# Performance work log

Measured on AMD Instinct MI355X. Metric: run time of the kernel, lower is better.

The kernel has to match this reference:

```python
import jax, jax.numpy as jnp
import numpy as np
import math

B, S, HID, H = 2, 1024, 512, 8
D = HID // H  # 64
EPS = 1e-24


def setup_inputs() -> dict:
    key = jax.random.key(0)
    ks = jax.random.split(key, 12)
    s = 0.02
    return {
        "input_tensor": jax.random.normal(ks[0], (B, S, HID), dtype=jnp.float32),
        "attention_mask": jnp.zeros((B, 1, S, S), dtype=jnp.float32),
        # Linear weights stored as [in, out] (y = x @ W + b)
        "Wq": jax.random.normal(ks[1], (HID, HID), dtype=jnp.float32) * s,
        "bq": jnp.zeros((HID,), dtype=jnp.float32),
        "Wk": jax.random.normal(ks[2], (HID, HID), dtype=jnp.float32) * s,
        "bk": jnp.zeros((HID,), dtype=jnp.float32),
        "Wv": jax.random.normal(ks[3], (HID, HID), dtype=jnp.float32) * s,
        "bv": jnp.zeros((HID,), dtype=jnp.float32),
        # order_affine: Linear(2*D, 1)
        "order_w": jax.random.normal(ks[4], (2 * D,), dtype=jnp.float32) * s,
        "order_b": jnp.zeros((), dtype=jnp.float32),
        # distance_affine: Linear(2*D, 1)
        "dist_w": jax.random.normal(ks[5], (2 * D,), dtype=jnp.float32) * s,
        "dist_b": jnp.zeros((), dtype=jnp.float32),
        "scalar": jax.random.normal(ks[6], (1,), dtype=jnp.float32),
    }


def _heads(x):  # [B,S,HID] -> [B,H,S,D]
    return x.reshape(B, S, H, D).transpose(0, 2, 1, 3)


def reference(input_tensor, attention_mask, Wq, bq, Wk, bk, Wv, bv,
              order_w, order_b, dist_w, dist_b, scalar):
    scale = math.sqrt(D)

    mixed_q = input_tensor @ Wq + bq            # [B,S,HID]
    mixed_k = input_tensor @ Wk + bk
    mixed_v = input_tensor @ Wv + bv

    qh = _heads(mixed_q)                        # [B,H,S,D]
    kh = _heads(mixed_k)
    vh = _heads(mixed_v)

    scores = jnp.einsum('bhid,bhjd->bhij', qh, kh)   # [B,H,S,S]
    origin_scores = scores

    # --- order bias: sigmoid(affine(cat(q_i, k_j))) decomposed (same math,
    # avoids materializing the [B,H,S,S,2D] concat the torch code builds) ---
    q_ord = jnp.einsum('bhid,d->bhi', qh, order_w[:D])    # [B,H,S]
    k_ord = jnp.einsum('bhjd,d->bhj', kh, order_w[D:])
    pr_order = jax.nn.sigmoid(q_ord[..., :, None] + k_ord[..., None, :] + order_b)
    gd_order = jnp.triu(jnp.ones((S, S), dtype=scores.dtype), k=1)  # 1 where j>i
    error_order = (jnp.log(pr_order + EPS) * gd_order
                   + jnp.log(1.0 - pr_order + EPS) * (1.0 - gd_order))

    # --- distance bias ---
    idx = jnp.arange(S)
    gd_distance = jnp.log(jnp.abs(idx[None, :] - idx[:, None]).astype(scores.dtype) + 1.0)
    q_dst = jnp.einsum('bhid,d->bhi', qh, dist_w[:D])
    k_dst = jnp.einsum('bhjd,d->bhj', kh, dist_w[D:])
    pr_distance = q_dst[..., :, None] + k_dst[..., None, :] + dist_b   # [B,H,S,S]
    error_distance = -jnp.square(gd_distance - pr_distance) * jnp.square(scalar[0]) * 0.5

    adj_scores = scores + error_order + error_distance

    def _probs(sc):
        return jax.nn.softmax(sc / scale + attention_mask, axis=-1)

    attention_probs = _probs(adj_scores)
    origin_attention_probs = _probs(origin_scores)

    return (mixed_q, mixed_k, vh, attention_probs, origin_attention_probs)
```

## Files before the change

### kernel.cpp

```cpp
#include <hip/hip_runtime.h>
#include <math.h>

#define Sdim 1024
#define HIDdim 512
#define Hnum 8
#define Ddim 64

typedef __attribute__((ext_vector_type(4))) float f32x4;
typedef __attribute__((ext_vector_type(8))) short short8;
typedef __attribute__((ext_vector_type(4))) unsigned short ushort4v;

static __device__ __forceinline__ unsigned short f2bf(float x) {
    union { float f; unsigned u; } v; v.f = x;
    unsigned r = v.u + 0x7fffu + ((v.u >> 16) & 1u);
    return (unsigned short)(r >> 16);
}

__global__ __launch_bounds__(256) void qkv_gemm(
    const float* __restrict__ X,
    const float* __restrict__ Wq, const float* __restrict__ bq,
    const float* __restrict__ Wk, const float* __restrict__ bk,
    const float* __restrict__ Wv, const float* __restrict__ bv,
    float* __restrict__ outq, float* __restrict__ outk, float* __restrict__ outv)
{
    __shared__ unsigned short Ws[64][72];
    __shared__ unsigned short Xs[64][72];

    const int mb = blockIdx.x;
    const int nb = blockIdx.y;
    const int which = nb >> 3;
    const int n0 = (nb & 7) * 64;
    const float* __restrict__ W    = (which == 0) ? Wq : (which == 1) ? Wk : Wv;
    const float* __restrict__ bias = (which == 0) ? bq : (which == 1) ? bk : bv;

    const int t    = threadIdx.x;
    const int lane = t & 63;
    const int w    = t >> 6;
    const int g    = lane >> 4;
    const int c    = lane & 15;
    const int m0r  = mb * 64;

    f32x4 acc[4];
#pragma unroll
    for (int f = 0; f < 4; ++f) { f32x4 z = {0.f, 0.f, 0.f, 0.f}; acc[f] = z; }

    for (int kt = 0; kt < 512; kt += 64) {
        __syncthreads();
        {
            const int row = t >> 2, kb = (t & 3) * 16;
            const float* __restrict__ src = &X[(size_t)(m0r + row) * HIDdim + kt + kb];
#pragma unroll
            for (int i = 0; i < 4; ++i) {
                const f32x4 v = *(const f32x4*)&src[4 * i];
                ushort4v p;
                p.x = f2bf(v.x); p.y = f2bf(v.y); p.z = f2bf(v.z); p.w = f2bf(v.w);
                *(ushort4v*)&Xs[row][kb + 4 * i] = p;
            }
        }
#pragma unroll
        for (int p = 0; p < 4; ++p) {
            const int kr   = p * 16 + (t >> 4);
            const int nloc = (t & 15) * 4;
            const f32x4 v = *(const f32x4*)&W[(size_t)(kt + kr) * HIDdim + n0 + nloc];
            Ws[nloc + 0][kr] = f2bf(v.x);
            Ws[nloc + 1][kr] = f2bf(v.y);
            Ws[nloc + 2][kr] = f2bf(v.z);
            Ws[nloc + 3][kr] = f2bf(v.w);
        }
        __syncthreads();
        const short8 a0 = *(const short8*)&Ws[w * 16 + c][g * 8];
        const short8 a1 = *(const short8*)&Ws[w * 16 + c][32 + g * 8];
#pragma unroll
        for (int f = 0; f < 4; ++f) {
            const short8 b0 = *(const short8*)&Xs[f * 16 + c][g * 8];
            const short8 b1 = *(const short8*)&Xs[f * 16 + c][32 + g * 8];
            acc[f] = __builtin_amdgcn_mfma_f32_16x16x32_bf16(a0, b0, acc[f], 0, 0, 0);
            acc[f] = __builtin_amdgcn_mfma_f32_16x16x32_bf16(a1, b1, acc[f], 0, 0, 0);
        }
    }

    const int nql = w * 16 + g * 4;
    const f32x4 bb = *(const f32x4*)&bias[n0 + nql];
#pragma unroll
    for (int f = 0; f < 4; ++f) {
        const int m = m0r + f * 16 + c;
        f32x4 v = acc[f] + bb;
        if (which == 2) {
            const int b = m >> 10, s = m & 1023;
            const int h = nb & 7;
            *(f32x4*)&outv[((((size_t)b * Hnum + h) * Sdim) + s) * Ddim + nql] = v;
        } else {
            float* __restrict__ o = (which == 0) ? outq : outk;
            *(f32x4*)&o[(size_t)m * HIDdim + n0 + nql] = v;
        }
    }
}

__global__ __launch_bounds__(256) void prep_kernel(
    const float* __restrict__ mq, const float* __restrict__ mk,
    const float* __restrict__ order_w, const float* __restrict__ dist_w,
    unsigned short* __restrict__ qbf, unsigned short* __restrict__ kbf,
    float* __restrict__ qog, float* __restrict__ qdg,
    float* __restrict__ kog, float* __restrict__ kdg)
{
    const int tg  = blockIdx.x * 256 + threadIdx.x;
    const int row = tg >> 3;
    const int dc8 = (tg & 7) * 8;
    const int bh  = row >> 10, s = row & 1023;
    const int b   = bh >> 3,   h = bh & 7;
    const size_t src = ((size_t)b * Sdim + s) * HIDdim + h * Ddim + dc8;

    const f32x4 ow0 = *(const f32x4*)&order_w[dc8];
    const f32x4 ow1 = *(const f32x4*)&order_w[dc8 + 4];
    const f32x4 dw0 = *(const f32x4*)&dist_w[dc8];
    const f32x4 dw1 = *(const f32x4*)&dist_w[dc8 + 4];
    const f32x4 owk0 = *(const f32x4*)&order_w[Ddim + dc8];
    const f32x4 owk1 = *(const f32x4*)&order_w[Ddim + dc8 + 4];
    const f32x4 dwk0 = *(const f32x4*)&dist_w[Ddim + dc8];
    const f32x4 dwk1 = *(const f32x4*)&dist_w[Ddim + dc8 + 4];

    {
        const f32x4 v0 = *(const f32x4*)&mq[src];
        const f32x4 v1 = *(const f32x4*)&mq[src + 4];
        float po = v0.x * ow0.x + v0.y * ow0.y + v0.z * ow0.z + v0.w * ow0.w
                 + v1.x * ow1.x + v1.y * ow1.y + v1.z * ow1.z + v1.w * ow1.w;
        float pd = v0.x * dw0.x + v0.y * dw0.y + v0.z * dw0.z + v0.w * dw0.w
                 + v1.x * dw1.x + v1.y * dw1.y + v1.z * dw1.z + v1.w * dw1.w;
#pragma unroll
        for (int o = 1; o < 8; o <<= 1) { po += __shfl_xor(po, o); pd += __shfl_xor(pd, o); }
        if ((tg & 7) == 0) { qog[row] = po; qdg[row] = pd; }
        ushort4v p0, p1;
        p0.x = f2bf(v0.x); p0.y = f2bf(v0.y); p0.z = f2bf(v0.z); p0.w = f2bf(v0.w);
        p1.x = f2bf(v1.x); p1.y = f2bf(v1.y); p1.z = f2bf(v1.z); p1.w = f2bf(v1.w);
        *(ushort4v*)&qbf[(size_t)row * Ddim + dc8]     = p0;
        *(ushort4v*)&qbf[(size_t)row * Ddim + dc8 + 4] = p1;
    }
    {
        const f32x4 v0 = *(const f32x4*)&mk[src];
        const f32x4 v1 = *(const f32x4*)&mk[src + 4];
        float po = v0.x * owk0.x + v0.y * owk0.y + v0.z * owk0.z + v0.w * owk0.w
                 + v1.x * owk1.x + v1.y * owk1.y + v1.z * owk1.z + v1.w * owk1.w;
        float pd = v0.x * dwk0.x + v0.y * dwk0.y + v0.z * dwk0.z + v0.w * dwk0.w
                 + v1.x * dwk1.x + v1.y * dwk1.y + v1.z * dwk1.z + v1.w * dwk1.w;
#pragma unroll
        for (int o = 1; o < 8; o <<= 1) { po += __shfl_xor(po, o); pd += __shfl_xor(pd, o); }
        if ((tg & 7) == 0) { kog[row] = po; kdg[row] = pd; }
        ushort4v p0, p1;
        p0.x = f2bf(v0.x); p0.y = f2bf(v0.y); p0.z = f2bf(v0.z); p0.w = f2bf(v0.w);
        p1.x = f2bf(v1.x); p1.y = f2bf(v1.y); p1.z = f2bf(v1.z); p1.w = f2bf(v1.w);
        *(ushort4v*)&kbf[(size_t)row * Ddim + dc8]     = p0;
        *(ushort4v*)&kbf[(size_t)row * Ddim + dc8 + 4] = p1;
    }
}

__global__ __launch_bounds__(512, 6) void attn_kernel(
    const unsigned short* __restrict__ qbf, const unsigned short* __restrict__ kbf,
    const float* __restrict__ qog, const float* __restrict__ qdg,
    const float* __restrict__ kog, const float* __restrict__ kdg,
    const float* __restrict__ mask,
    const float* __restrict__ order_b_p, const float* __restrict__ dist_b_p,
    const float* __restrict__ scalar_p,
    float* __restrict__ out_adj, float* __restrict__ out_orig)
{
    __shared__ float ps[16][524];
    __shared__ float gdl[Sdim];
    __shared__ float red_s[16][8];

    const int t    = threadIdx.x;
    const int lane = t & 63;
    const int w    = t >> 6;
    const int g    = lane >> 4;
    const int c    = lane & 15;

    const int blk = blockIdx.x;
    const int ib  = blk & 63;
    const int bh  = blk >> 6;
    const int b   = bh >> 3;
    const int i0  = ib * 16;
    const int i   = i0 + c;

    const float order_b = order_b_p[0];
    const float dist_b  = dist_b_p[0];
    const float sc      = scalar_p[0];
    const float sc2h    = 0.5f * sc * sc;
    const float mscale  = 0.125f;

    {
        const int idx = t * 2;
        gdl[idx]     = __logf((float)idx + 1.0f);
        gdl[idx + 1] = __logf((float)idx + 2.0f);
    }
    __syncthreads();

    const size_t hbase = (size_t)bh * Sdim;
    const size_t qrow  = (hbase + i) * Ddim;
    const short8 qf0 = *(const short8*)&qbf[qrow + g * 8];
    const short8 qf1 = *(const short8*)&qbf[qrow + 32 + g * 8];

    f32x4 acc[8];
#pragma unroll
    for (int it = 0; it < 8; ++it) { f32x4 z = {0.f, 0.f, 0.f, 0.f}; acc[it] = z; }

#pragma unroll
    for (int it = 0; it < 8; ++it) {
        const size_t kr = (hbase + it * 128 + w * 16 + c) * Ddim;
        const short8 kf0 = *(const short8*)&kbf[kr + g * 8];
        const short8 kf1 = *(const short8*)&kbf[kr + 32 + g * 8];
        acc[it] = __builtin_amdgcn_mfma_f32_16x16x32_bf16(kf0, qf0, acc[it], 0, 0, 0);
        acc[it] = __builtin_amdgcn_mfma_f32_16x16x32_bf16(kf1, qf1, acc[it], 0, 0, 0);
    }

    const size_t obase = (size_t)bh * Sdim * Sdim;
    const float* __restrict__ mrow = &mask[((size_t)b * Sdim + i) * Sdim];

    float s0 = 0.0f;
#pragma unroll
    for (int it = 0; it < 8; ++it) {
        const int j0 = it * 128 + w * 16 + g * 4;
        const f32x4 mk4 = *(const f32x4*)&mrow[j0];
        f32x4 e;
#pragma unroll
        for (int r = 0; r < 4; ++r) e[r] = __expf(fmaf(acc[it][r], mscale, mk4[r]));
        acc[it] = e;
        s0 += e[0] + e[1] + e[2] + e[3];
    }
    s0 += __shfl_xor(s0, 16);
    s0 += __shfl_xor(s0, 32);
    if (lane < 16) red_s[lane][w] = s0;
    __syncthreads();
    f32x4 ra = *(const f32x4*)&red_s[c][0];
    f32x4 rb = *(const f32x4*)&red_s[c][4];
    const float inv0 = __builtin_amdgcn_rcpf(ra[0] + ra[1] + ra[2] + ra[3]
                                           + rb[0] + rb[1] + rb[2] + rb[3]);

#pragma unroll
    for (int hf = 0; hf < 2; ++hf) {
        __syncthreads();
#pragma unroll
        for (int it = 0; it < 4; ++it) {
            const int colw = it * 128 + w * 16 + g * 4;
            f32x4 p = acc[hf * 4 + it] * inv0;
            *(f32x4*)&ps[c][colw] = p;
        }
        __syncthreads();
        float* __restrict__ dst = out_orig + obase + (size_t)i0 * Sdim + hf * 512;
#pragma unroll
        for (int n = 0; n < 4; ++n) {
            const int row = 2 * w + (n >> 1);
            const int col = (n & 1) * 256 + lane * 4;
            const f32x4 v = *(const f32x4*)&ps[row][col];
            *(f32x4*)&dst[(size_t)row * Sdim + col] = v;
        }
    }

    const float qo = qog[hbase + i] + order_b;
    const float qd = qdg[hbase + i] + dist_b;
    float s1 = 0.0f;
#pragma unroll
    for (int it = 0; it < 8; ++it) {
        const int j0 = it * 128 + w * 16 + g * 4;
        const f32x4 ko4 = *(const f32x4*)&kog[hbase + j0];
        const f32x4 kd4 = *(const f32x4*)&kdg[hbase + j0];
        f32x4 p = acc[it];
#pragma unroll
        for (int r = 0; r < 4; ++r) {
            const int j = j0 + r;
            const float z    = qo + ko4[r];
            const float targ = (j > i) ? -z : z;
            const float u    = 1.0f + __expf(targ);
            const int   dl   = (i > j) ? (i - j) : (j - i);
            const float df   = gdl[dl] - (qd + kd4[r]);
            const float eD   = __expf(-0.125f * fmaf(sc2h * df, df, __logf(u)));
            p[r] *= eD;
            s1 += p[r];
        }
        acc[it] = p;
    }
    s1 += __shfl_xor(s1, 16);
    s1 += __shfl_xor(s1, 32);
    __syncthreads();
    if (lane < 16) red_s[lane][w] = s1;
    __syncthreads();
    ra = *(const f32x4*)&red_s[c][0];
    rb = *(const f32x4*)&red_s[c][4];
    const float inv1 = __builtin_amdgcn_rcpf(ra[0] + ra[1] + ra[2] + ra[3]
                                           + rb[0] + rb[1] + rb[2] + rb[3]);

#pragma unroll
    for (int hf = 0; hf < 2; ++hf) {
        __syncthreads();
#pragma unroll
        for (int it = 0; it < 4; ++it) {
            const int colw = it * 128 + w * 16 + g * 4;
            f32x4 p = acc[hf * 4 + it] * inv1;
            *(f32x4*)&ps[c][colw] = p;
        }
        __syncthreads();
        float* __restrict__ dst = out_adj + obase + (size_t)i0 * Sdim + hf * 512;
#pragma unroll
        for (int n = 0; n < 4; ++n) {
            const int row = 2 * w + (n >> 1);
            const int col = (n & 1) * 256 + lane * 4;
            const f32x4 v = *(const f32x4*)&ps[row][col];
            *(f32x4*)&dst[(size_t)row * Sdim + col] = v;
        }
    }
}

extern "C" void kernel_launch(void* const* d_in, const int* in_sizes, int n_in,
                              void* d_out, int out_size, void* d_ws, size_t ws_size,
                              hipStream_t stream) {
    const float* X    = (const float*)d_in[0];
    const float* mask = (const float*)d_in[1];
    const float* Wq   = (const float*)d_in[2];
    const float* bq   = (const float*)d_in[3];
    const float* Wk   = (const float*)d_in[4];
    const float* bk   = (const float*)d_in[5];
    const float* Wv   = (const float*)d_in[6];
    const float* bv   = (const float*)d_in[7];
    const float* ow   = (const float*)d_in[8];
    const float* ob   = (const float*)d_in[9];
    const float* dw   = (const float*)d_in[10];
    const float* db   = (const float*)d_in[11];
    const float* sc   = (const float*)d_in[12];

    float* out     = (float*)d_out;
    float* outq    = out;
    float* outk    = out + 1048576;
    float* outv    = out + 2097152;
    float* outadj  = out + 3145728;
    float* outorig = out + 19922944;

    unsigned short* qbf = (unsigned short*)d_ws;
    unsigned short* kbf = qbf + 16384 * 64;
    float* qog = (float*)(kbf + 16384 * 64);
    float* qdg = qog + 16384;
    float* kog = qdg + 16384;
    float* kdg = kog + 16384;

    qkv_gemm<<<dim3(32, 24), 256, 0, stream>>>(X, Wq, bq, Wk, bk, Wv, bv,
                                               outq, outk, outv);
    prep_kernel<<<dim3(512), 256, 0, stream>>>(outq, outk, ow, dw,
                                               qbf, kbf, qog, qdg, kog, kdg);
    attn_kernel<<<dim3(1024), 512, 0, stream>>>(qbf, kbf, qog, qdg, kog, kdg,
                                                mask, ob, db, sc,
                                                outadj, outorig);
}
```

Before: 79.04 us.

## Transpose attention MFMA orientation and shuffle-pack W transpose into LDS

The QKV GEMM now packs bf16 pairs and uses cross-lane shuffles, so each lane writes two 32-bit words into the transposed W tile instead of four scattered 16-bit LDS stores. The attention kernel swaps the MFMA operand order so each lane holds four query rows for one key column. The mask, bias and softmax reductions are reorganised to match, with row sums taken over 16 lanes via shuffles and the per-row scalars loaded as four values per lane. Occupancy hint drops from 6 to 4 waves; mask and kog/kdg reads become scalar per-element loads, and the LDS stores into ps become scalar rather than vectorised.

```diff
diff --git a/kernel.cpp b/kernel.cpp
--- a/kernel.cpp
+++ b/kernel.cpp
@@ -39,6 +39,8 @@
     const int g    = lane >> 4;
     const int c    = lane & 15;
     const int m0r  = mb * 64;
+    const int rr   = g;
+    const int nq   = c * 4;
 
     f32x4 acc[4];
 #pragma unroll
@@ -59,13 +61,28 @@
         }
 #pragma unroll
         for (int p = 0; p < 4; ++p) {
-            const int kr   = p * 16 + (t >> 4);
-            const int nloc = (t & 15) * 4;
-            const f32x4 v = *(const f32x4*)&W[(size_t)(kt + kr) * HIDdim + n0 + nloc];
-            Ws[nloc + 0][kr] = f2bf(v.x);
-            Ws[nloc + 1][kr] = f2bf(v.y);
-            Ws[nloc + 2][kr] = f2bf(v.z);
-            Ws[nloc + 3][kr] = f2bf(v.w);
+            const int kr = p * 16 + w * 4 + rr;
+            const f32x4 v = *(const f32x4*)&W[(size_t)(kt + kr) * HIDdim + n0 + nq];
+            unsigned lo = (unsigned)f2bf(v.x) | ((unsigned)f2bf(v.y) << 16);
+            unsigned hi = (unsigned)f2bf(v.z) | ((unsigned)f2bf(v.w) << 16);
+            const unsigned plo = __shfl_xor((int)lo, 32);
+            const unsigned phi = __shfl_xor((int)hi, 32);
+            const unsigned lo1 = (rr & 2) ? phi : lo;
+            const unsigned hi1 = (rr & 2) ? hi : plo;
+            const unsigned pl = __shfl_xor((int)lo1, 16);
+            const unsigned ph = __shfl_xor((int)hi1, 16);
+            unsigned lo2, hi2;
+            if (!(rr & 1)) {
+                lo2 = (lo1 & 0xFFFFu) | (pl << 16);
+                hi2 = (hi1 & 0xFFFFu) | (ph << 16);
+            } else {
+                lo2 = (pl >> 16) | (lo1 & 0xFFFF0000u);
+                hi2 = (ph >> 16) | (hi1 & 0xFFFF0000u);
+            }
+            const int kbase = p * 16 + w * 4;
+            unsigned* dst = (unsigned*)&Ws[nq + rr][kbase];
+            dst[0] = lo2;
+            dst[1] = hi2;
         }
         __syncthreads();
         const short8 a0 = *(const short8*)&Ws[w * 16 + c][g * 8];
@@ -153,7 +170,7 @@
     }
 }
 
-__global__ __launch_bounds__(512, 6) void attn_kernel(
+__global__ __launch_bounds__(512, 4) void attn_kernel(
     const unsigned short* __restrict__ qbf, const unsigned short* __restrict__ kbf,
     const float* __restrict__ qog, const float* __restrict__ qdg,
     const float* __restrict__ kog, const float* __restrict__ kdg,
@@ -177,7 +194,6 @@
     const int bh  = blk >> 6;
     const int b   = bh >> 3;
     const int i0  = ib * 16;
-    const int i   = i0 + c;
 
     const float order_b = order_b_p[0];
     const float dist_b  = dist_b_p[0];
@@ -193,7 +209,7 @@
     __syncthreads();
 
     const size_t hbase = (size_t)bh * Sdim;
-    const size_t qrow  = (hbase + i) * Ddim;
+    const size_t qrow = (hbase + i0 + c) * Ddim;
     const short8 qf0 = *(const short8*)&qbf[qrow + g * 8];
     const short8 qf1 = *(const short8*)&qbf[qrow + 32 + g * 8];
 
@@ -206,41 +222,53 @@
         const size_t kr = (hbase + it * 128 + w * 16 + c) * Ddim;
         const short8 kf0 = *(const short8*)&kbf[kr + g * 8];
         const short8 kf1 = *(const short8*)&kbf[kr + 32 + g * 8];
-        acc[it] = __builtin_amdgcn_mfma_f32_16x16x32_bf16(kf0, qf0, acc[it], 0, 0, 0);
-        acc[it] = __builtin_amdgcn_mfma_f32_16x16x32_bf16(kf1, qf1, acc[it], 0, 0, 0);
+        acc[it] = __builtin_amdgcn_mfma_f32_16x16x32_bf16(qf0, kf0, acc[it], 0, 0, 0);
+        acc[it] = __builtin_amdgcn_mfma_f32_16x16x32_bf16(qf1, kf1, acc[it], 0, 0, 0);
     }
 
     const size_t obase = (size_t)bh * Sdim * Sdim;
-    const float* __restrict__ mrow = &mask[((size_t)b * Sdim + i) * Sdim];
-
-    float s0 = 0.0f;
+    const int jw = w * 16 + c;
+
+    float s0[4] = {0.f, 0.f, 0.f, 0.f};
 #pragma unroll
     for (int it = 0; it < 8; ++it) {
-        const int j0 = it * 128 + w * 16 + g * 4;
-        const f32x4 mk4 = *(const f32x4*)&mrow[j0];
-        f32x4 e;
-#pragma unroll
-        for (int r = 0; r < 4; ++r) e[r] = __expf(fmaf(acc[it][r], mscale, mk4[r]));
-        acc[it] = e;
-        s0 += e[0] + e[1] + e[2] + e[3];
-    }
-    s0 += __shfl_xor(s0, 16);
-    s0 += __shfl_xor(s0, 32);
-    if (lane < 16) red_s[lane][w] = s0;
+        const int j = it * 128 + jw;
+#pragma unroll
+        for (int r = 0; r < 4; ++r) {
+            const float mkv = mask[((size_t)b * Sdim + i0 + g * 4 + r) * Sdim + j];
+            const float e = __expf(fmaf(acc[it][r], mscale, mkv));
+            acc[it][r] = e;
+            s0[r] += e;
+        }
+    }
+#pragma unroll
+    for (int r = 0; r < 4; ++r) {
+#pragma unroll
+        for (int o = 1; o < 16; o <<= 1) s0[r] += __shfl_xor(s0[r], o);
+    }
+    if (c == 0) {
+#pragma unroll
+        for (int r = 0; r < 4; ++r) red_s[g * 4 + r][w] = s0[r];
+    }
     __syncthreads();
-    f32x4 ra = *(const f32x4*)&red_s[c][0];
-    f32x4 rb = *(const f32x4*)&red_s[c][4];
-    const float inv0 = __builtin_amdgcn_rcpf(ra[0] + ra[1] + ra[2] + ra[3]
-                                           + rb[0] + rb[1] + rb[2] + rb[3]);
+    float inv0[4];
+#pragma unroll
+    for (int r = 0; r < 4; ++r) {
+        const f32x4 ra = *(const f32x4*)&red_s[g * 4 + r][0];
+        const f32x4 rb = *(const f32x4*)&red_s[g * 4 + r][4];
+        inv0[r] = __builtin_amdgcn_rcpf(ra[0] + ra[1] + ra[2] + ra[3]
+                                      + rb[0] + rb[1] + rb[2] + rb[3]);
+    }
 
 #pragma unroll
     for (int hf = 0; hf < 2; ++hf) {
         __syncthreads();
 #pragma unroll
-        for (int it = 0; it < 4; ++it) {
-            const int colw = it * 128 + w * 16 + g * 4;
-            f32x4 p = acc[hf * 4 + it] * inv0;
-            *(f32x4*)&ps[c][colw] = p;
+        for (int itl = 0; itl < 4; ++itl) {
+            const int colw = itl * 128 + jw;
+#pragma unroll
+            for (int r = 0; r < 4; ++r)
+                ps[g * 4 + r][colw] = acc[hf * 4 + itl][r] * inv0[r];
         }
         __syncthreads();
         float* __restrict__ dst = out_orig + obase + (size_t)i0 * Sdim + hf * 512;
@@ -253,47 +281,61 @@
         }
     }
 
-    const float qo = qog[hbase + i] + order_b;
-    const float qd = qdg[hbase + i] + dist_b;
-    float s1 = 0.0f;
+    float qo[4], qd[4];
+#pragma unroll
+    for (int r = 0; r < 4; ++r) {
+        qo[r] = qog[hbase + i0 + g * 4 + r] + order_b;
+        qd[r] = qdg[hbase + i0 + g * 4 + r] + dist_b;
+    }
+    float s1[4] = {0.f, 0.f, 0.f, 0.f};
 #pragma unroll
     for (int it = 0; it < 8; ++it) {
-        const int j0 = it * 128 + w * 16 + g * 4;
-        const f32x4 ko4 = *(const f32x4*)&kog[hbase + j0];
-        const f32x4 kd4 = *(const f32x4*)&kdg[hbase + j0];
-        f32x4 p = acc[it];
+        const int j = it * 128 + jw;
+        const float ko = kog[hbase + j];
+        const float kd = kdg[hbase + j];
 #pragma unroll
         for (int r = 0; r < 4; ++r) {
-            const int j = j0 + r;
-            const float z    = qo + ko4[r];
+            const int i = i0 + g * 4 + r;
+            const float z    = qo[r] + ko;
             const float targ = (j > i) ? -z : z;
             const float u    = 1.0f + __expf(targ);
             const int   dl   = (i > j) ? (i - j) : (j - i);
-            const float df   = gdl[dl] - (qd + kd4[r]);
+            const float df   = gdl[dl] - (qd[r] + kd);
             const float eD   = __expf(-0.125f * fmaf(sc2h * df, df, __logf(u)));
-            p[r] *= eD;
-            s1 += p[r];
-        }
-        acc[it] = p;
-    }
-    s1 += __shfl_xor(s1, 16);
-    s1 += __shfl_xor(s1, 32);
+            const float p    = acc[it][r] * eD;
+            acc[it][r] = p;
+            s1[r] += p;
+        }
+    }
+#pragma unroll
+    for (int r = 0; r < 4; ++r) {
+#pragma unroll
+        for (int o = 1; o < 16; o <<= 1) s1[r] += __shfl_xor(s1[r], o);
+    }
     __syncthreads();
-    if (lane < 16) red_s[lane][w] = s1;
+    if (c == 0) {
+#pragma unroll
+        for (int r = 0; r < 4; ++r) red_s[g * 4 + r][w] = s1[r];
+    }
     __syncthreads();
-    ra = *(const f32x4*)&red_s[c][0];
-    rb = *(const f32x4*)&red_s[c][4];
-    const float inv1 = __builtin_amdgcn_rcpf(ra[0] + ra[1] + ra[2] + ra[3]
-                                           + rb[0] + rb[1] + rb[2] + rb[3]);
+    float inv1[4];
+#pragma unroll
+    for (int r = 0; r < 4; ++r) {
+        const f32x4 ra = *(const f32x4*)&red_s[g * 4 + r][0];
+        const f32x4 rb = *(const f32x4*)&red_s[g * 4 + r][4];
+        inv1[r] = __builtin_amdgcn_rcpf(ra[0] + ra[1] + ra[2] + ra[3]
+                                      + rb[0] + rb[1] + rb[2] + rb[3]);
+    }
 
 #pragma unroll
     for (int hf = 0; hf < 2; ++hf) {
         __syncthreads();
 #pragma unroll
-        for (int it = 0; it < 4; ++it) {
-            const int colw = it * 128 + w * 16 + g * 4;
-            f32x4 p = acc[hf * 4 + it] * inv1;
-            *(f32x4*)&ps[c][colw] = p;
+        for (int itl = 0; itl < 4; ++itl) {
+            const int colw = itl * 128 + jw;
+#pragma unroll
+            for (int r = 0; r < 4; ++r)
+                ps[g * 4 + r][colw] = acc[hf * 4 + itl][r] * inv1[r];
         }
         __syncthreads();
         float* __restrict__ dst = out_adj + obase + (size_t)i0 * Sdim + hf * 512;
```

Result: no change. 77.50 us (-1.9%).
